# Performance work log

Hardware: AMD Instinct MI355X
Metric: run time of the kernel (lower is better)

## Reference

```python
import jax, jax.numpy as jnp
import numpy as np

T, B, I, H, U = 256, 64, 512, 1024, 8  # time, batch, input, hidden, unit_input_size
EPS = 1e-5  # BatchNorm1d default eps


def setup_inputs() -> dict:
    key = jax.random.key(0)
    ks = jax.random.split(key, 8)
    x = jax.random.normal(ks[0], (T, B, I), dtype=jnp.float32)
    Wzx = jax.random.normal(ks[1], (H, I), dtype=jnp.float32) * (1.0 / np.sqrt(I))
    Whx = jax.random.normal(ks[2], (U * H, I), dtype=jnp.float32) * (np.sqrt(2.0 / I))
    Uz = jax.random.normal(ks[3], (H, H), dtype=jnp.float32) * (1.0 / np.sqrt(H))
    Uh = jax.random.normal(ks[4], (H, H), dtype=jnp.float32) * (1.0 / np.sqrt(H))
    b_unit = jnp.zeros((U * H,), dtype=jnp.float32)
    # block-diagonal matrix: row h has ones in columns [h*U, (h+1)*U)
    Wh_in_mask = jnp.kron(jnp.eye(H, dtype=jnp.float32), jnp.ones((1, U), dtype=jnp.float32))
    Wh_in = Wh_in_mask  # init value is exactly the block-diagonal ones matrix
    gz = jnp.ones((H,), dtype=jnp.float32)
    bz = jnp.zeros((H,), dtype=jnp.float32)
    gh = jnp.ones((H,), dtype=jnp.float32)
    bh = jnp.zeros((H,), dtype=jnp.float32)
    return {"x": x, "Wzx": Wzx, "Whx": Whx, "Uz": Uz, "Uh": Uh,
            "b_unit": b_unit, "Wh_in": Wh_in, "gz": gz, "bz": bz,
            "gh": gh, "bh": bh, "Wh_in_mask": Wh_in_mask}


def _bn(y, g, b):
    # training-mode BatchNorm1d: per-step batch stats over the batch dim, biased var
    mu = jnp.mean(y, axis=0)
    var = jnp.var(y, axis=0)
    return (y - mu) * jax.lax.rsqrt(var + EPS) * g + b


def reference(x, Wzx, Whx, Uz, Uh, b_unit, Wh_in, gz, bz, gh, bh, Wh_in_mask):
    # precompute input projections for all timesteps (math-equivalent, batched GEMM)
    zx = jnp.einsum('tbi,hi->tbh', x, Wzx)                 # [T,B,H]
    hx = jnp.einsum('tbi,ui->tbu', x, Whx) + b_unit        # [T,B,U*H]
    Wm = Wh_in * Wh_in_mask                                # [H,U*H] block-diag

    def step(h, inp):
        zx_t, hx_t = inp
        z = jax.nn.sigmoid(_bn(zx_t, gz, bz) + h @ Uz.T)           # [B,H]
        h_in = jax.nn.relu(hx_t)                                    # [B,U*H]
        h_ungated = jax.nn.relu(_bn(h_in @ Wm.T, gh, bh) + h @ Uh.T)
        h_new = z * h + (1.0 - z) * h_ungated
        return h_new, h_new

    h0 = jnp.zeros((x.shape[1], Uz.shape[0]), dtype=x.dtype)
    h_final, timeseries = jax.lax.scan(step, h0, (zx, hx))
    return timeseries, h_final
```

## Files before the change

### kernel.cpp

```cpp
#include <hip/hip_runtime.h>
#include <hip/hip_bf16.h>

#define T_DIM 256
#define B_DIM 64
#define I_DIM 512
#define H_DIM 1024
#define U_DIM 8
#define BN_EPS 1e-5f
#define BH (B_DIM * H_DIM)
#define NCHUNK 64
#define TILES_PER_CHUNK 80
#define NTILES 5120

typedef __bf16 bf16x8 __attribute__((ext_vector_type(8)));
typedef float f32x4 __attribute__((ext_vector_type(4)));
typedef int i32x4 __attribute__((ext_vector_type(4)));
typedef unsigned short u16;
typedef u16 u16x4 __attribute__((ext_vector_type(4)));
typedef unsigned long long u64;
using bf16 = __hip_bfloat16;


__global__ void k_cvt4(const float* __restrict__ in, u16* __restrict__ out, int n4) {
    int i = blockIdx.x * blockDim.x + threadIdx.x;
    int stride = gridDim.x * blockDim.x;
    for (; i < n4; i += stride) {
        f32x4 v = *reinterpret_cast<const f32x4*>(in + (size_t)i * 4);
        u16x4 o;
#pragma unroll
        for (int j = 0; j < 4; ++j)
            o[j] = __bfloat16_as_ushort(__float2bfloat16(v[j]));
        *reinterpret_cast<u16x4*>(out + (size_t)i * 4) = o;
    }
}

__global__ void k_pack_uzuh(const float* __restrict__ Uz, const float* __restrict__ Uh,
                            u16* __restrict__ out) {
    int i = blockIdx.x * 256 + threadIdx.x;
    int stride = gridDim.x * 256;
    int n4 = 2 * H_DIM * H_DIM / 4;
    for (; i < n4; i += stride) {
        int c = i * 4;
        int n = c >> 10, k = c & 1023;
        const float* src = (n < H_DIM) ? (Uz + (size_t)n * H_DIM + k)
                                       : (Uh + (size_t)(n - H_DIM) * H_DIM + k);
        f32x4 v = *reinterpret_cast<const f32x4*>(src);
        u16x4 o;
#pragma unroll
        for (int j = 0; j < 4; ++j)
            o[j] = __bfloat16_as_ushort(__float2bfloat16(v[j]));
        *reinterpret_cast<u16x4*>(out + c) = o;
    }
}

__global__ void k_wdiag(const float* __restrict__ Wh_in, const float* __restrict__ mask,
                        float* __restrict__ wdiag) {
    int idx = blockIdx.x * 256 + threadIdx.x;
    if (idx < H_DIM * U_DIM) {
        int h = idx >> 3;
        size_t col = (size_t)h * (H_DIM * U_DIM) + idx;
        wdiag[idx] = Wh_in[col] * mask[col];
    }
}

__device__ __forceinline__ bf16x8 cvt8(const float* p) {
    f32x4 a = *reinterpret_cast<const f32x4*>(p);
    f32x4 b = *reinterpret_cast<const f32x4*>(p + 4);
    union { u16 u[8]; bf16x8 v; } r;
#pragma unroll
    for (int j = 0; j < 4; ++j) {
        r.u[j]     = __bfloat16_as_ushort(__float2bfloat16(a[j]));
        r.u[4 + j] = __bfloat16_as_ushort(__float2bfloat16(b[j]));
    }
    return r.v;
}


__global__ __launch_bounds__(512, 2) void k_mega(
    const float* __restrict__ x,
    const bf16* __restrict__ wzx, const bf16* __restrict__ whx,
    const float* __restrict__ b_unit, const float* __restrict__ wdiag,
    const float* __restrict__ gzp, const float* __restrict__ bzp,
    const float* __restrict__ ghp, const float* __restrict__ bhp,
    const bf16* __restrict__ uzuh,
    bf16* bnz, bf16* bnh,
    bf16* hb0, bf16* hb1,
    float* out, unsigned* flags, unsigned* done) {

    __shared__ float smem[4096];
    int tid = threadIdx.x;

    if (blockIdx.x < 64) {
        int lane = tid & 63, w = tid >> 6;
        int cg = w >> 1, kq = w & 1;
        int r15 = lane & 15, kseg = lane >> 4;
        int cohort = blockIdx.x & 3, blk = blockIdx.x >> 2;
        int h0 = blk * 64 + cg * 16;
        int batch = cohort * 16 + r15;
        int hd0 = blk * 64 + cg * 16 + kseg * 4;

        unsigned* fbase = flags + (size_t)cohort * 1024;
        unsigned* myflag = fbase + (size_t)(blk * 4 + cg) * 16;
        unsigned* depflag = fbase + (size_t)(kq * 32 + (lane & 31)) * 16;

        bf16x8 aZ[16], aH[16];
        {
            const bf16* azb = uzuh + (size_t)(h0 + r15) * H_DIM + kq * 512 + kseg * 8;
            const bf16* ahb = azb + (size_t)H_DIM * H_DIM;
#pragma unroll
            for (int i = 0; i < 16; ++i) {
                aZ[i] = *reinterpret_cast<const bf16x8*>(azb + i * 32);
                aH[i] = *reinterpret_cast<const bf16x8*>(ahb + i * 32);
            }
        }

#define REDX(par, zh, c, l, j) smem[(par) * 2048 + (zh) * 1024 + (c) * 256 + (l) * 4 + (j)]

        f32x4 hreg = {};
        float bzv[4], bhv[4];

        for (int t = 0; t < T_DIM; ++t) {
            const bf16* hbc = (t & 1) ? hb1 : hb0;
            bf16* hbn = (t & 1) ? hb0 : hb1;

            if ((t & 3) == 0 && kq == 0) {
                while (__hip_atomic_load(&done[t >> 2], __ATOMIC_RELAXED,
                                         __HIP_MEMORY_SCOPE_AGENT) < (unsigned)TILES_PER_CHUNK)
                    __builtin_amdgcn_s_sleep(8);
                asm volatile("" ::: "memory");
                u16x4 vz = *reinterpret_cast<const u16x4*>(
                    bnz + (size_t)t * BH + (size_t)batch * H_DIM + hd0);
                u16x4 vh = *reinterpret_cast<const u16x4*>(
                    bnh + (size_t)t * BH + (size_t)batch * H_DIM + hd0);
#pragma unroll
                for (int j = 0; j < 4; ++j) {
                    bzv[j] = __bfloat162float(__ushort_as_bfloat16(vz[j]));
                    bhv[j] = __bfloat162float(__ushort_as_bfloat16(vh[j]));
                }
            }

            if (t > 0) {
                while (true) {
                    unsigned v = __hip_atomic_load(depflag, __ATOMIC_RELAXED,
                                                   __HIP_MEMORY_SCOPE_AGENT);
                    if (!__any(v < (unsigned)t)) break;
                    __builtin_amdgcn_s_sleep(1);
                }
            }

            i32x4 hv[16];
            const bf16* hp = hbc + (size_t)batch * H_DIM + kq * 512 + kseg * 8;
#pragma unroll
            for (int i = 0; i < 16; ++i)
                asm volatile("global_load_dwordx4 %0, %1, off sc0 sc1"
                             : "=v"(hv[i]) : "v"(hp + i * 32));
            asm volatile("s_waitcnt vmcnt(0)" ::: "memory");
            __builtin_amdgcn_sched_barrier(0);

            f32x4 accZ = {}, accH = {};
#pragma unroll
            for (int i = 0; i < 16; ++i) {
                bf16x8 b = __builtin_bit_cast(bf16x8, hv[i]);
                accZ = __builtin_amdgcn_mfma_f32_16x16x32_bf16(aZ[i], b, accZ, 0, 0, 0);
                accH = __builtin_amdgcn_mfma_f32_16x16x32_bf16(aH[i], b, accH, 0, 0, 0);
            }

            int par = t & 1;
            if (kq == 1) {
                *reinterpret_cast<f32x4*>(&REDX(par, 0, cg, lane, 0)) = accZ;
                *reinterpret_cast<f32x4*>(&REDX(par, 1, cg, lane, 0)) = accH;
            }
            __syncthreads();

            if (kq == 0) {
                accZ += *reinterpret_cast<const f32x4*>(&REDX(par, 0, cg, lane, 0));
                accH += *reinterpret_cast<const f32x4*>(&REDX(par, 1, cg, lane, 0));
#pragma unroll
                for (int j = 0; j < 4; ++j) {
                    float z = 1.f / (1.f + __expf(-(bzv[j] + accZ[j])));
                    float hu = fmaxf(bhv[j] + accH[j], 0.f);
                    hreg[j] = z * hreg[j] + (1.f - z) * hu;
                }
                if (t < T_DIM - 1) {
                    u16x4 o;
#pragma unroll
                    for (int j = 0; j < 4; ++j)
                        o[j] = __bfloat16_as_ushort(__float2bfloat16(hreg[j]));
                    u64 old = __hip_atomic_exchange(
                        (u64*)(hbn + (size_t)batch * H_DIM + hd0),
                        __builtin_bit_cast(u64, o),
                        __ATOMIC_RELAXED, __HIP_MEMORY_SCOPE_AGENT);
                    asm volatile("" :: "v"(old));
                    asm volatile("s_waitcnt vmcnt(0)" ::: "memory");
                    if (lane == 0)
                        __hip_atomic_store(myflag, (unsigned)(t + 1),
                                           __ATOMIC_RELAXED, __HIP_MEMORY_SCOPE_AGENT);
                }
                *reinterpret_cast<f32x4*>(out + (size_t)t * BH + (size_t)batch * H_DIM + hd0) = hreg;
                if (t == T_DIM - 1)
                    *reinterpret_cast<f32x4*>(out + (size_t)T_DIM * BH + (size_t)batch * H_DIM + hd0) = hreg;
                if (t + 1 < T_DIM && ((t + 1) & 3) != 0) {
                    u16x4 vz = *reinterpret_cast<const u16x4*>(
                        bnz + (size_t)(t + 1) * BH + (size_t)batch * H_DIM + hd0);
                    u16x4 vh = *reinterpret_cast<const u16x4*>(
                        bnh + (size_t)(t + 1) * BH + (size_t)batch * H_DIM + hd0);
#pragma unroll
                    for (int j = 0; j < 4; ++j) {
                        bzv[j] = __bfloat162float(__ushort_as_bfloat16(vz[j]));
                        bhv[j] = __bfloat162float(__ushort_as_bfloat16(vh[j]));
                    }
                }
            }
        }
        return;
    }

    {
        int q = blockIdx.x - 64;
        int sub = tid >> 8;
        int ltid = tid & 255;
        int lane = ltid & 63;
        int mq = ltid >> 6;
        int r15 = lane & 15;
        int kseg = lane >> 4;
        float* sm = smem + sub * 2048;
#define SB(st, wd, tt, col) sm[(st) * 1024 + (wd) * 256 + (tt) * 64 + (col)]

        for (int g = q * 2 + sub; g < NTILES; g += 384) {
            int c = g / TILES_PER_CHUNK;
            int s = g % TILES_PER_CHUNK;
            int t0 = c * 4;

            if (s < 16) {
                int h0 = s * 64;
                const float* xbase = x + (size_t)(t0 * B_DIM + mq * 16 + r15) * I_DIM + kseg * 8;
                f32x4 acc[4][4] = {};
                for (int kk = 0; kk < I_DIM; kk += 32) {
                    bf16x8 b[4];
#pragma unroll
                    for (int nf = 0; nf < 4; ++nf)
                        b[nf] = *reinterpret_cast<const bf16x8*>(
                            wzx + (size_t)(h0 + nf * 16 + r15) * I_DIM + kk + kseg * 8);
#pragma unroll
                    for (int tt = 0; tt < 4; ++tt) {
                        bf16x8 a = cvt8(xbase + (size_t)tt * B_DIM * I_DIM + kk);
#pragma unroll
                        for (int nf = 0; nf < 4; ++nf)
                            acc[tt][nf] = __builtin_amdgcn_mfma_f32_16x16x32_bf16(
                                a, b[nf], acc[tt][nf], 0, 0, 0);
                    }
                }
#pragma unroll
                for (int tt = 0; tt < 4; ++tt)
#pragma unroll
                    for (int nf = 0; nf < 4; ++nf) {
                        float sv = acc[tt][nf][0] + acc[tt][nf][1] + acc[tt][nf][2] + acc[tt][nf][3];
                        float s2 = acc[tt][nf][0] * acc[tt][nf][0] + acc[tt][nf][1] * acc[tt][nf][1] +
                                   acc[tt][nf][2] * acc[tt][nf][2] + acc[tt][nf][3] * acc[tt][nf][3];
                        sv += __shfl_xor(sv, 16); sv += __shfl_xor(sv, 32);
                        s2 += __shfl_xor(s2, 16); s2 += __shfl_xor(s2, 32);
                        if (lane < 16) {
                            SB(0, mq, tt, nf * 16 + r15) = sv;
                            SB(1, mq, tt, nf * 16 + r15) = s2;
                        }
                    }
                __syncthreads();
                int bb = mq * 16 + kseg * 4;
#pragma unroll
                for (int tt = 0; tt < 4; ++tt)
#pragma unroll
                    for (int nf = 0; nf < 4; ++nf) {
                        int col = nf * 16 + r15;
                        float sv = SB(0, 0, tt, col) + SB(0, 1, tt, col) + SB(0, 2, tt, col) + SB(0, 3, tt, col);
                        float s2 = SB(1, 0, tt, col) + SB(1, 1, tt, col) + SB(1, 2, tt, col) + SB(1, 3, tt, col);
                        float mu = sv * (1.f / B_DIM);
                        float var = s2 * (1.f / B_DIM) - mu * mu;
                        int h = h0 + col;
                        float sc = rsqrtf(var + BN_EPS) * gzp[h];
                        float sh = bzp[h] - mu * sc;
#pragma unroll
                        for (int j = 0; j < 4; ++j)
                            bnz[(size_t)((t0 + tt) * B_DIM + bb + j) * H_DIM + h] =
                                __float2bfloat16(acc[tt][nf][j] * sc + sh);
                    }
            } else {
                int h0 = (s - 16) * 16;
                int u0 = h0 * U_DIM;
                const float* xbase = x + (size_t)(t0 * B_DIM + mq * 16 + r15) * I_DIM + kseg * 8;
                f32x4 acc[4][8] = {};
                for (int kk = 0; kk < I_DIM; kk += 32) {
                    bf16x8 b[8];
#pragma unroll
                    for (int nf = 0; nf < 8; ++nf)
                        b[nf] = *reinterpret_cast<const bf16x8*>(
                            whx + (size_t)(u0 + nf * 16 + r15) * I_DIM + kk + kseg * 8);
#pragma unroll
                    for (int tt = 0; tt < 4; ++tt) {
                        bf16x8 a = cvt8(xbase + (size_t)tt * B_DIM * I_DIM + kk);
#pragma unroll
                        for (int nf = 0; nf < 8; ++nf)
                            acc[tt][nf] = __builtin_amdgcn_mfma_f32_16x16x32_bf16(
                                a, b[nf], acc[tt][nf], 0, 0, 0);
                    }
                }
                int uloc = r15 & 7;
#pragma unroll
                for (int nf = 0; nf < 8; ++nf) {
                    int ucol = u0 + nf * 16 + r15;
                    float wd = wdiag[ucol];
                    float bu = b_unit[ucol];
#pragma unroll
                    for (int tt = 0; tt < 4; ++tt)
#pragma unroll
                        for (int j = 0; j < 4; ++j) {
                            float v = fmaxf(acc[tt][nf][j] + bu, 0.f) * wd;
                            v += __shfl_xor(v, 1);
                            v += __shfl_xor(v, 2);
                            v += __shfl_xor(v, 4);
                            acc[tt][nf][j] = v;
                        }
                }
#pragma unroll
                for (int tt = 0; tt < 4; ++tt)
#pragma unroll
                    for (int nf = 0; nf < 8; ++nf) {
                        float sv = 0.f, s2 = 0.f;
                        if (uloc == 0) {
#pragma unroll
                            for (int j = 0; j < 4; ++j) {
                                sv += acc[tt][nf][j];
                                s2 += acc[tt][nf][j] * acc[tt][nf][j];
                            }
                        }
                        sv += __shfl_xor(sv, 16); sv += __shfl_xor(sv, 32);
                        s2 += __shfl_xor(s2, 16); s2 += __shfl_xor(s2, 32);
                        if (lane == 0 || lane == 8) {
                            int col = nf * 2 + (r15 >> 3);
                            SB(0, mq, tt, col) = sv;
                            SB(1, mq, tt, col) = s2;
                        }
                    }
                __syncthreads();
                int bb = mq * 16 + kseg * 4;
#pragma unroll
                for (int tt = 0; tt < 4; ++tt)
#pragma unroll
                    for (int nf = 0; nf < 8; ++nf) {
                        int col = nf * 2 + (r15 >> 3);
                        float sv = SB(0, 0, tt, col) + SB(0, 1, tt, col) + SB(0, 2, tt, col) + SB(0, 3, tt, col);
                        float s2 = SB(1, 0, tt, col) + SB(1, 1, tt, col) + SB(1, 2, tt, col) + SB(1, 3, tt, col);
                        float mu = sv * (1.f / B_DIM);
                        float var = s2 * (1.f / B_DIM) - mu * mu;
                        int h = h0 + col;
                        float sc = rsqrtf(var + BN_EPS) * ghp[h];
                        float sh = bhp[h] - mu * sc;
                        if (uloc == 0) {
#pragma unroll
                            for (int j = 0; j < 4; ++j)
                                bnh[(size_t)((t0 + tt) * B_DIM + bb + j) * H_DIM + h] =
                                    __float2bfloat16(acc[tt][nf][j] * sc + sh);
                        }
                    }
            }
            __syncthreads();
            if (ltid == 0)
                __hip_atomic_fetch_add(&done[c], 1u, __ATOMIC_RELEASE, __HIP_MEMORY_SCOPE_AGENT);
        }
    }
}

#define OFF_WZX   ((size_t)16777216)
#define OFF_WHX   ((size_t)17825792)
#define OFF_UZUH  ((size_t)26214400)
#define OFF_WDIAG ((size_t)30408704)
#define OFF_BNZ   ((size_t)30441472)
#define OFF_BNH   ((size_t)63995904)
#define OFF_BAR   ((size_t)97550336)
#define OFF_DONE  ((size_t)97615872)
#define OFF_HB0   ((size_t)98074624)
#define OFF_HB1   ((size_t)98205696)

extern "C" void kernel_launch(void* const* d_in, const int* in_sizes, int n_in,
                              void* d_out, int out_size, void* d_ws, size_t ws_size,
                              hipStream_t stream) {
    const float* x      = (const float*)d_in[0];
    const float* Wzx    = (const float*)d_in[1];
    const float* Whx    = (const float*)d_in[2];
    const float* Uz     = (const float*)d_in[3];
    const float* Uh     = (const float*)d_in[4];
    const float* b_unit = (const float*)d_in[5];
    const float* Wh_in  = (const float*)d_in[6];
    const float* gz     = (const float*)d_in[7];
    const float* bz     = (const float*)d_in[8];
    const float* gh     = (const float*)d_in[9];
    const float* bh     = (const float*)d_in[10];
    const float* mask   = (const float*)d_in[11];

    char* ws = (char*)d_ws;
    bf16*     wzx_b = (bf16*)(ws + OFF_WZX);
    bf16*     whx_b = (bf16*)(ws + OFF_WHX);
    bf16*     uzuh  = (bf16*)(ws + OFF_UZUH);
    float*    wdiag = (float*)(ws + OFF_WDIAG);
    bf16*     bnz   = (bf16*)(ws + OFF_BNZ);
    bf16*     bnh   = (bf16*)(ws + OFF_BNH);
    unsigned* flags = (unsigned*)(ws + OFF_BAR);
    unsigned* done  = (unsigned*)(ws + OFF_DONE);
    bf16*     hb0   = (bf16*)(ws + OFF_HB0);
    bf16*     hb1   = (bf16*)(ws + OFF_HB1);

    float* out = (float*)d_out;

    k_cvt4<<<512, 256, 0, stream>>>(Wzx, (u16*)wzx_b, H_DIM * I_DIM / 4);
    k_cvt4<<<2048, 256, 0, stream>>>(Whx, (u16*)whx_b, U_DIM * H_DIM * I_DIM / 4);
    k_pack_uzuh<<<2048, 256, 0, stream>>>(Uz, Uh, (u16*)uzuh);
    k_wdiag<<<(H_DIM * U_DIM + 255) / 256, 256, 0, stream>>>(Wh_in, mask, wdiag);

    hipMemsetAsync(hb0, 0, (size_t)BH * sizeof(bf16), stream);
    hipMemsetAsync(flags, 0, 16384, stream);
    hipMemsetAsync(done, 0, 4096, stream);

    k_mega<<<256, 512, 0, stream>>>(x, wzx_b, whx_b, b_unit, wdiag,
                                    gz, bz, gh, bh, uzuh,
                                    bnz, bnh, hb0, hb1, out, flags, done);
}
```

Measured before the change: 1.918 ms.

## Replace per-step flag handshake with sign-bit tags embedded in hidden state

```diff
diff --git a/kernel.cpp b/kernel.cpp
--- a/kernel.cpp
+++ b/kernel.cpp
@@ -63,6 +63,11 @@
     }
 }
 
+__global__ void k_init_tag(u64* __restrict__ p, int n) {
+    int i = blockIdx.x * 256 + threadIdx.x;
+    if (i < n) p[i] = 0x8000800080008000ull;
+}
+
 __device__ __forceinline__ bf16x8 cvt8(const float* p) {
     f32x4 a = *reinterpret_cast<const f32x4*>(p);
     f32x4 b = *reinterpret_cast<const f32x4*>(p + 4);
@@ -85,7 +90,7 @@
     const bf16* __restrict__ uzuh,
     bf16* bnz, bf16* bnh,
     bf16* hb0, bf16* hb1,
-    float* out, unsigned* flags, unsigned* done) {
+    float* out, unsigned* done) {
 
     __shared__ float smem[4096];
     int tid = threadIdx.x;
@@ -99,10 +104,6 @@
         int batch = cohort * 16 + r15;
         int hd0 = blk * 64 + cg * 16 + kseg * 4;
 
-        unsigned* fbase = flags + (size_t)cohort * 1024;
-        unsigned* myflag = fbase + (size_t)(blk * 4 + cg) * 16;
-        unsigned* depflag = fbase + (size_t)(kq * 32 + (lane & 31)) * 16;
-
         bf16x8 aZ[16], aH[16];
         {
             const bf16* azb = uzuh + (size_t)(h0 + r15) * H_DIM + kq * 512 + kseg * 8;
@@ -119,43 +120,53 @@
         f32x4 hreg = {};
         float bzv[4], bhv[4];
 
+        if (kq == 0) {
+            while (__hip_atomic_load(&done[0], __ATOMIC_RELAXED,
+                                     __HIP_MEMORY_SCOPE_AGENT) < (unsigned)TILES_PER_CHUNK)
+                __builtin_amdgcn_s_sleep(8);
+            asm volatile("" ::: "memory");
+            u16x4 vz = *reinterpret_cast<const u16x4*>(bnz + (size_t)batch * H_DIM + hd0);
+            u16x4 vh = *reinterpret_cast<const u16x4*>(bnh + (size_t)batch * H_DIM + hd0);
+#pragma unroll
+            for (int j = 0; j < 4; ++j) {
+                bzv[j] = __bfloat162float(__ushort_as_bfloat16(vz[j]));
+                bhv[j] = __bfloat162float(__ushort_as_bfloat16(vh[j]));
+            }
+        }
+
         for (int t = 0; t < T_DIM; ++t) {
             const bf16* hbc = (t & 1) ? hb1 : hb0;
             bf16* hbn = (t & 1) ? hb0 : hb1;
 
-            if ((t & 3) == 0 && kq == 0) {
-                while (__hip_atomic_load(&done[t >> 2], __ATOMIC_RELAXED,
-                                         __HIP_MEMORY_SCOPE_AGENT) < (unsigned)TILES_PER_CHUNK)
-                    __builtin_amdgcn_s_sleep(8);
-                asm volatile("" ::: "memory");
-                u16x4 vz = *reinterpret_cast<const u16x4*>(
-                    bnz + (size_t)t * BH + (size_t)batch * H_DIM + hd0);
-                u16x4 vh = *reinterpret_cast<const u16x4*>(
-                    bnh + (size_t)t * BH + (size_t)batch * H_DIM + hd0);
-#pragma unroll
-                for (int j = 0; j < 4; ++j) {
-                    bzv[j] = __bfloat162float(__ushort_as_bfloat16(vz[j]));
-                    bhv[j] = __bfloat162float(__ushort_as_bfloat16(vh[j]));
-                }
-            }
-
-            if (t > 0) {
-                while (true) {
-                    unsigned v = __hip_atomic_load(depflag, __ATOMIC_RELAXED,
-                                                   __HIP_MEMORY_SCOPE_AGENT);
-                    if (!__any(v < (unsigned)t)) break;
-                    __builtin_amdgcn_s_sleep(1);
-                }
-            }
+            int rt = t ? (((t - 1) >> 1) & 1) : 1;
+            int expect = rt << 15;
 
             i32x4 hv[16];
             const bf16* hp = hbc + (size_t)batch * H_DIM + kq * 512 + kseg * 8;
-#pragma unroll
-            for (int i = 0; i < 16; ++i)
-                asm volatile("global_load_dwordx4 %0, %1, off sc0 sc1"
-                             : "=v"(hv[i]) : "v"(hp + i * 32));
-            asm volatile("s_waitcnt vmcnt(0)" ::: "memory");
+            int tries = 0;
+            while (true) {
+#pragma unroll
+                for (int i = 0; i < 16; ++i)
+                    asm volatile("global_load_dwordx4 %0, %1, off sc0 sc1"
+                                 : "=v"(hv[i]) : "v"(hp + i * 32));
+                asm volatile("s_waitcnt vmcnt(0)" ::: "memory");
+                unsigned bad = 0;
+#pragma unroll
+                for (int i = 0; i < 16; ++i) {
+                    bad |= (unsigned)((hv[i][0] ^ expect) & 0x8000);
+                    bad |= (unsigned)((hv[i][2] ^ expect) & 0x8000);
+                }
+                if (!__any(bad != 0u)) break;
+                if (++tries > 2) __builtin_amdgcn_s_sleep(1);
+            }
             __builtin_amdgcn_sched_barrier(0);
+
+#pragma unroll
+            for (int i = 0; i < 16; ++i) {
+#pragma unroll
+                for (int c = 0; c < 4; ++c)
+                    hv[i][c] &= 0x7FFF7FFF;
+            }
 
             f32x4 accZ = {}, accH = {};
 #pragma unroll
@@ -182,24 +193,27 @@
                     hreg[j] = z * hreg[j] + (1.f - z) * hu;
                 }
                 if (t < T_DIM - 1) {
+                    unsigned ptag = (unsigned)((t >> 1) & 1) << 15;
                     u16x4 o;
 #pragma unroll
                     for (int j = 0; j < 4; ++j)
-                        o[j] = __bfloat16_as_ushort(__float2bfloat16(hreg[j]));
+                        o[j] = (u16)(__bfloat16_as_ushort(__float2bfloat16(hreg[j])) | ptag);
                     u64 old = __hip_atomic_exchange(
                         (u64*)(hbn + (size_t)batch * H_DIM + hd0),
                         __builtin_bit_cast(u64, o),
                         __ATOMIC_RELAXED, __HIP_MEMORY_SCOPE_AGENT);
                     asm volatile("" :: "v"(old));
-                    asm volatile("s_waitcnt vmcnt(0)" ::: "memory");
-                    if (lane == 0)
-                        __hip_atomic_store(myflag, (unsigned)(t + 1),
-                                           __ATOMIC_RELAXED, __HIP_MEMORY_SCOPE_AGENT);
                 }
                 *reinterpret_cast<f32x4*>(out + (size_t)t * BH + (size_t)batch * H_DIM + hd0) = hreg;
                 if (t == T_DIM - 1)
                     *reinterpret_cast<f32x4*>(out + (size_t)T_DIM * BH + (size_t)batch * H_DIM + hd0) = hreg;
-                if (t + 1 < T_DIM && ((t + 1) & 3) != 0) {
+                if (t + 1 < T_DIM) {
+                    if (((t + 1) & 3) == 0) {
+                        while (__hip_atomic_load(&done[(t + 1) >> 2], __ATOMIC_RELAXED,
+                                                 __HIP_MEMORY_SCOPE_AGENT) < (unsigned)TILES_PER_CHUNK)
+                            __builtin_amdgcn_s_sleep(2);
+                        asm volatile("" ::: "memory");
+                    }
                     u16x4 vz = *reinterpret_cast<const u16x4*>(
                         bnz + (size_t)(t + 1) * BH + (size_t)batch * H_DIM + hd0);
                     u16x4 vh = *reinterpret_cast<const u16x4*>(
@@ -375,7 +389,6 @@
 #define OFF_WDIAG ((size_t)30408704)
 #define OFF_BNZ   ((size_t)30441472)
 #define OFF_BNH   ((size_t)63995904)
-#define OFF_BAR   ((size_t)97550336)
 #define OFF_DONE  ((size_t)97615872)
 #define OFF_HB0   ((size_t)98074624)
 #define OFF_HB1   ((size_t)98205696)
@@ -403,7 +416,6 @@
     float*    wdiag = (float*)(ws + OFF_WDIAG);
     bf16*     bnz   = (bf16*)(ws + OFF_BNZ);
     bf16*     bnh   = (bf16*)(ws + OFF_BNH);
-    unsigned* flags = (unsigned*)(ws + OFF_BAR);
     unsigned* done  = (unsigned*)(ws + OFF_DONE);
     bf16*     hb0   = (bf16*)(ws + OFF_HB0);
     bf16*     hb1   = (bf16*)(ws + OFF_HB1);
@@ -415,11 +427,11 @@
     k_pack_uzuh<<<2048, 256, 0, stream>>>(Uz, Uh, (u16*)uzuh);
     k_wdiag<<<(H_DIM * U_DIM + 255) / 256, 256, 0, stream>>>(Wh_in, mask, wdiag);
 
-    hipMemsetAsync(hb0, 0, (size_t)BH * sizeof(bf16), stream);
-    hipMemsetAsync(flags, 0, 16384, stream);
+    k_init_tag<<<128, 256, 0, stream>>>((u64*)hb0, BH / 4);
+    k_init_tag<<<128, 256, 0, stream>>>((u64*)hb1, BH / 4);
     hipMemsetAsync(done, 0, 4096, stream);
 
     k_mega<<<256, 512, 0, stream>>>(x, wzx_b, whx_b, b_unit, wdiag,
                                     gz, bz, gh, bh, uzuh,
-                                    bnz, bnh, hb0, hb1, out, flags, done);
-}
+                                    bnz, bnh, hb0, hb1, out, done);
+}
```

New measurement: 3.454 ms. +80.1%, slower.
